# Kernel optimization log

Measured on AMD Instinct MI355X. Metric: run time of the kernel, lower is better.

## Reference

```python
import jax, jax.numpy as jnp
import numpy as np

N_TOKENS = 4096
HIDDEN = 2048
INTER = 1024
N_EXPERTS = 8          # routed experts
ZERO_EXPERTS = 2       # Longcat zero-computation (identity) experts
TOP_K = 2
ROUTED_SCALING = 2.5


def setup_inputs() -> dict:
    key = jax.random.key(0)
    k1, k2, k3, k4 = jax.random.split(key, 4)
    hidden_states = jax.random.normal(k1, (N_TOKENS, HIDDEN), dtype=jnp.float32)
    router_w = jax.random.normal(k2, (N_EXPERTS + ZERO_EXPERTS, HIDDEN), dtype=jnp.float32) * 0.02
    correction_bias = jnp.zeros((N_EXPERTS + ZERO_EXPERTS,), dtype=jnp.float32)
    # torch Linear weight layout [out, in]: gate_up [E, 2I, H], down [E, H, I]
    w_gate_up = jax.random.normal(k3, (N_EXPERTS, 2 * INTER, HIDDEN), dtype=jnp.float32) * 0.02
    w_down = jax.random.normal(k4, (N_EXPERTS, HIDDEN, INTER), dtype=jnp.float32) * 0.02
    return {
        'hidden_states': hidden_states,
        'router_w': router_w,
        'correction_bias': correction_bias,
        'w_gate_up': w_gate_up,
        'w_down': w_down,
    }


def reference(hidden_states, router_w, correction_bias, w_gate_up, w_down):
    x = hidden_states  # [N, H]
    # ---- router gemm (fp32, like dsv3_router_gemm) ----
    logits = jnp.einsum('nh,eh->ne', x.astype(jnp.float32), router_w)  # [N, E+Z]
    scores = jax.nn.sigmoid(logits)
    # biased top-k selection (sglang biased topk, renormalize=False)
    _, topk_idx = jax.lax.top_k(scores + correction_bias[None, :], TOP_K)  # [N, K]
    topk_w = jnp.take_along_axis(scores, topk_idx, axis=1)  # raw sigmoid scores
    # ---- combine weights per expert ----
    onehot = jax.nn.one_hot(topk_idx, N_EXPERTS + ZERO_EXPERTS, dtype=topk_w.dtype)  # [N,K,E+Z]
    combine = jnp.einsum('nke,nk->ne', onehot, topk_w)  # [N, E+Z]
    combine_real = combine[:, :N_EXPERTS]               # [N, E]
    w_zero = combine[:, N_EXPERTS:].sum(axis=-1)        # [N] identity-expert weight
    # ---- expert FFN (silu(gate) * up -> down), dense over experts ----
    gu = jnp.einsum('nh,efh->enf', x, w_gate_up)        # [E, N, 2I]
    gate, up = gu[..., :INTER], gu[..., INTER:]
    h = jax.nn.silu(gate) * up                          # [E, N, I]
    y = jnp.einsum('eni,ehi->enh', h, w_down)           # [E, N, H]
    out = jnp.einsum('enh,ne->nh', y, combine_real.astype(y.dtype))
    out = out + w_zero[:, None].astype(out.dtype) * x   # zero experts = identity
    return out * ROUTED_SCALING
```

## Files before the change

kernel.cpp:

```cpp
#include <hip/hip_runtime.h>
#include <cstdint>
#include <cstddef>

#define N_TOKENS 4096
#define HIDDEN   2048
#define INTER    1024
#define NE       8
#define NE_TOT   10
#define SCALE    2.5f

typedef short v8s __attribute__((ext_vector_type(8)));
typedef float v4f __attribute__((ext_vector_type(4)));

static __device__ inline int imin(int a, int b) { return a < b ? a : b; }

__device__ inline unsigned short f2bf(float f) {
  unsigned int u = __float_as_uint(f);
  u += 0x7fffu + ((u >> 16) & 1u);
  return (unsigned short)(u >> 16);
}

__device__ inline void gld_lds16(const void* g, void* l) {
  __builtin_amdgcn_global_load_lds(
      (const __attribute__((address_space(1))) unsigned int*)g,
      (__attribute__((address_space(3))) unsigned int*)l, 16, 0, 0);
}

__global__ void init_kernel(int* counts) {
  if (threadIdx.x < NE) counts[threadIdx.x] = 0;
}

__global__ __launch_bounds__(256) void cvt_kernel(const float* __restrict__ src,
                                                  unsigned short* __restrict__ dst,
                                                  int n8) {
  int i = blockIdx.x * 256 + threadIdx.x;
  if (i >= n8) return;
  size_t b = (size_t)i * 8;
  float4 a0 = *(const float4*)(src + b);
  float4 a1 = *(const float4*)(src + b + 4);
  union { unsigned short u[8]; uint4 v; } r;
  r.u[0] = f2bf(a0.x); r.u[1] = f2bf(a0.y); r.u[2] = f2bf(a0.z); r.u[3] = f2bf(a0.w);
  r.u[4] = f2bf(a1.x); r.u[5] = f2bf(a1.y); r.u[6] = f2bf(a1.z); r.u[7] = f2bf(a1.w);
  *(uint4*)(dst + b) = r.v;
}

__global__ __launch_bounds__(256, 4) void router_kernel(
    const float* __restrict__ x, const float* __restrict__ rw,
    const float* __restrict__ bias, unsigned short* __restrict__ xb,
    int* __restrict__ counts, int* __restrict__ tok_list,
    float* __restrict__ tok_w, float* __restrict__ out) {
  int tid  = threadIdx.x;
  int lane = tid & 63;
  int wid  = tid >> 6;
  int n    = blockIdx.x * 4 + wid;

  const float* xr = x + (size_t)n * HIDDEN;
  float acc[NE_TOT];
#pragma unroll
  for (int e = 0; e < NE_TOT; e++) acc[e] = 0.f;

#pragma unroll 1
  for (int i = 0; i < 8; i++) {
    int k = (i * 64 + lane) * 4;
    float4 xv = *(const float4*)(xr + k);
#pragma unroll
    for (int e = 0; e < NE_TOT; e++) {
      float4 w = *(const float4*)(rw + (size_t)e * HIDDEN + k);
      acc[e] += xv.x * w.x + xv.y * w.y + xv.z * w.z + xv.w * w.w;
    }
  }
#pragma unroll
  for (int e = 0; e < NE_TOT; e++) {
    float v = acc[e];
#pragma unroll
    for (int off = 32; off > 0; off >>= 1) v += __shfl_xor(v, off, 64);
    acc[e] = v;
  }

  float sc[NE_TOT], sb[NE_TOT];
#pragma unroll
  for (int e = 0; e < NE_TOT; e++) {
    sc[e] = 1.f / (1.f + expf(-acc[e]));
    sb[e] = sc[e] + bias[e];
  }
  int i1 = 0;
  for (int e = 1; e < NE_TOT; e++) if (sb[e] > sb[i1]) i1 = e;
  int i2 = (i1 == 0) ? 1 : 0;
  for (int e = 0; e < NE_TOT; e++) if (e != i1 && sb[e] > sb[i2]) i2 = e;
  float wzero = 0.f;
  if (i1 >= NE) wzero += sc[i1];
  if (i2 >= NE) wzero += sc[i2];
  if (lane == 0) {
#pragma unroll
    for (int tt = 0; tt < 2; tt++) {
      int idx = tt == 0 ? i1 : i2;
      if (idx < NE) {
        int slot = atomicAdd(&counts[idx], 1);
        tok_list[idx * N_TOKENS + slot] = n;
        tok_w[idx * N_TOKENS + slot]    = SCALE * sc[idx];
      }
    }
  }
  float wz = SCALE * wzero;

#pragma unroll
  for (int i = 0; i < 8; i++) {
    int k = (i * 64 + lane) * 4;
    float4 xv = *(const float4*)(xr + k);
    ushort4 ob;
    ob.x = f2bf(xv.x); ob.y = f2bf(xv.y);
    ob.z = f2bf(xv.z); ob.w = f2bf(xv.w);
    *(ushort4*)(xb + (size_t)n * HIDDEN + k) = ob;
    float4 o;
    o.x = wz * xv.x; o.y = wz * xv.y; o.z = wz * xv.z; o.w = wz * xv.w;
    *(float4*)(out + (size_t)n * HIDDEN + k) = o;
  }
}

__global__ void offsets_kernel(const int* __restrict__ counts, int* __restrict__ offsets) {
  if (threadIdx.x == 0) {
    int s = 0;
    for (int e = 0; e < NE; e++) { offsets[e] = s; s += counts[e]; }
  }
}


__global__ __launch_bounds__(256, 2) void gateup_kernel(
    const unsigned short* __restrict__ xb, const unsigned short* __restrict__ wgu,
    const int* __restrict__ counts, const int* __restrict__ offsets,
    const int* __restrict__ tok_list, unsigned short* __restrict__ h_buf) {
  int jt = blockIdx.x;
  int mt = blockIdx.y;
  int e  = blockIdx.z;
  int count = counts[e];
  if (mt * 128 >= count) return;

  __shared__ unsigned short As[2][128 * 32];
  __shared__ unsigned short Bs[2][128 * 32];

  int tid  = threadIdx.x;
  int lane = tid & 63;
  int wm = (tid >> 7) & 1;
  int wn = (tid >> 6) & 1;

  int row0 = tid >> 2, row1 = row0 + 64;
  int col8 = (((tid & 3) ^ ((tid >> 3) & 3)) * 8);

  const int* tl = tok_list + e * N_TOKENS;
  int t0 = tl[imin(mt * 128 + row0, count - 1)];
  int t1 = tl[imin(mt * 128 + row1, count - 1)];
  const unsigned short* ag0 = xb + (size_t)t0 * HIDDEN + col8;
  const unsigned short* ag1 = xb + (size_t)t1 * HIDDEN + col8;

  int wn0 = row0 >> 6, wi0 = row0 & 63;
  int wn1 = row1 >> 6, wi1 = row1 & 63;
  int br0 = (wi0 < 32) ? (jt * 64 + wn0 * 32 + wi0) : (1024 + jt * 64 + wn0 * 32 + (wi0 - 32));
  int br1 = (wi1 < 32) ? (jt * 64 + wn1 * 32 + wi1) : (1024 + jt * 64 + wn1 * 32 + (wi1 - 32));
  const unsigned short* bbase = wgu + (size_t)e * (2 * INTER) * HIDDEN;
  const unsigned short* bg0 = bbase + (size_t)br0 * HIDDEN + col8;
  const unsigned short* bg1 = bbase + (size_t)br1 * HIDDEN + col8;

  v4f acc[4][4];
#pragma unroll
  for (int i = 0; i < 4; i++)
#pragma unroll
    for (int j = 0; j < 4; j++) acc[i][j] = v4f{0.f, 0.f, 0.f, 0.f};

  int mrow = wm * 64 + (lane & 15);
  int nrow = wn * 64 + (lane & 15);
  int kcol = (((lane >> 4) ^ ((lane >> 1) & 3)) * 8);

  gld_lds16(ag0, &As[0][(size_t)tid * 8]);
  gld_lds16(ag1, &As[0][2048 + (size_t)tid * 8]);
  gld_lds16(bg0, &Bs[0][(size_t)tid * 8]);
  gld_lds16(bg1, &Bs[0][2048 + (size_t)tid * 8]);
  ag0 += 32; ag1 += 32; bg0 += 32; bg1 += 32;
  __syncthreads();

  const int NK = HIDDEN / 32;
  for (int kt = 0; kt < NK; kt++) {
    int cur = kt & 1;
    if (kt + 1 < NK) {
      int nxt = cur ^ 1;
      gld_lds16(ag0, &As[nxt][(size_t)tid * 8]);
      gld_lds16(ag1, &As[nxt][2048 + (size_t)tid * 8]);
      gld_lds16(bg0, &Bs[nxt][(size_t)tid * 8]);
      gld_lds16(bg1, &Bs[nxt][2048 + (size_t)tid * 8]);
      ag0 += 32; ag1 += 32; bg0 += 32; bg1 += 32;
    }
    v8s a[4], b[4];
#pragma unroll
    for (int i = 0; i < 4; i++) a[i] = *(const v8s*)&As[cur][(mrow + i * 16) * 32 + kcol];
#pragma unroll
    for (int j = 0; j < 4; j++) b[j] = *(const v8s*)&Bs[cur][(nrow + j * 16) * 32 + kcol];
#pragma unroll
    for (int i = 0; i < 4; i++)
#pragma unroll
      for (int j = 0; j < 4; j++)
        acc[i][j] = __builtin_amdgcn_mfma_f32_16x16x32_bf16(a[i], b[j], acc[i][j], 0, 0, 0);
    __syncthreads();
  }

  int ocol  = lane & 15;
  int orow4 = (lane >> 4) * 4;
  int hoff  = offsets[e];
#pragma unroll
  for (int i = 0; i < 4; i++) {
#pragma unroll
    for (int r = 0; r < 4; r++) {
      int m = mt * 128 + wm * 64 + i * 16 + orow4 + r;
      if (m < count) {
        unsigned short* hrow = h_buf + (size_t)(hoff + m) * INTER;
#pragma unroll
        for (int j = 0; j < 2; j++) {
          float g = acc[i][j][r];
          float u = acc[i][j + 2][r];
          float hv = (g / (1.f + expf(-g))) * u;
          hrow[jt * 64 + wn * 32 + j * 16 + ocol] = f2bf(hv);
        }
      }
    }
  }
}

__global__ __launch_bounds__(256, 2) void down_kernel(
    const unsigned short* __restrict__ h_buf, const unsigned short* __restrict__ wd,
    const int* __restrict__ counts, const int* __restrict__ offsets,
    const int* __restrict__ tok_list, const float* __restrict__ tok_w,
    float* __restrict__ out) {
  int nt = blockIdx.x;
  int mt = blockIdx.y;
  int e  = blockIdx.z;
  int count = counts[e];
  if (mt * 128 >= count) return;

  __shared__ unsigned short As[2][128 * 32];
  __shared__ unsigned short Bs[2][128 * 32];

  int tid  = threadIdx.x;
  int lane = tid & 63;
  int wm = (tid >> 7) & 1;
  int wn = (tid >> 6) & 1;

  int row0 = tid >> 2, row1 = row0 + 64;
  int col8 = (((tid & 3) ^ ((tid >> 3) & 3)) * 8);
  int hoff = offsets[e];

  const unsigned short* ag0 =
      h_buf + (size_t)(hoff + imin(mt * 128 + row0, count - 1)) * INTER + col8;
  const unsigned short* ag1 =
      h_buf + (size_t)(hoff + imin(mt * 128 + row1, count - 1)) * INTER + col8;
  const unsigned short* bbase = wd + (size_t)e * HIDDEN * INTER;
  const unsigned short* bg0 = bbase + (size_t)(nt * 128 + row0) * INTER + col8;
  const unsigned short* bg1 = bbase + (size_t)(nt * 128 + row1) * INTER + col8;

  v4f acc[4][4];
#pragma unroll
  for (int i = 0; i < 4; i++)
#pragma unroll
    for (int j = 0; j < 4; j++) acc[i][j] = v4f{0.f, 0.f, 0.f, 0.f};

  int mrow = wm * 64 + (lane & 15);
  int nrow = wn * 64 + (lane & 15);
  int kcol = (((lane >> 4) ^ ((lane >> 1) & 3)) * 8);

  gld_lds16(ag0, &As[0][(size_t)tid * 8]);
  gld_lds16(ag1, &As[0][2048 + (size_t)tid * 8]);
  gld_lds16(bg0, &Bs[0][(size_t)tid * 8]);
  gld_lds16(bg1, &Bs[0][2048 + (size_t)tid * 8]);
  ag0 += 32; ag1 += 32; bg0 += 32; bg1 += 32;
  __syncthreads();

  const int NK = INTER / 32;
  for (int kt = 0; kt < NK; kt++) {
    int cur = kt & 1;
    if (kt + 1 < NK) {
      int nxt = cur ^ 1;
      gld_lds16(ag0, &As[nxt][(size_t)tid * 8]);
      gld_lds16(ag1, &As[nxt][2048 + (size_t)tid * 8]);
      gld_lds16(bg0, &Bs[nxt][(size_t)tid * 8]);
      gld_lds16(bg1, &Bs[nxt][2048 + (size_t)tid * 8]);
      ag0 += 32; ag1 += 32; bg0 += 32; bg1 += 32;
    }
    v8s a[4], b[4];
#pragma unroll
    for (int i = 0; i < 4; i++) a[i] = *(const v8s*)&As[cur][(mrow + i * 16) * 32 + kcol];
#pragma unroll
    for (int j = 0; j < 4; j++) b[j] = *(const v8s*)&Bs[cur][(nrow + j * 16) * 32 + kcol];
#pragma unroll
    for (int i = 0; i < 4; i++)
#pragma unroll
      for (int j = 0; j < 4; j++)
        acc[i][j] = __builtin_amdgcn_mfma_f32_16x16x32_bf16(a[i], b[j], acc[i][j], 0, 0, 0);
    __syncthreads();
  }

  int ocol  = lane & 15;
  int orow4 = (lane >> 4) * 4;
#pragma unroll
  for (int i = 0; i < 4; i++) {
#pragma unroll
    for (int r = 0; r < 4; r++) {
      int m = mt * 128 + wm * 64 + i * 16 + orow4 + r;
      if (m < count) {
        int tok  = tok_list[e * N_TOKENS + m];
        float w  = tok_w[e * N_TOKENS + m];
        float* orow = out + (size_t)tok * HIDDEN + nt * 128 + wn * 64 + ocol;
#pragma unroll
        for (int j = 0; j < 4; j++) atomicAdd(orow + j * 16, acc[i][j][r] * w);
      }
    }
  }
}

extern "C" void kernel_launch(void* const* d_in, const int* in_sizes, int n_in,
                              void* d_out, int out_size, void* d_ws, size_t ws_size,
                              hipStream_t stream) {
  const float* x   = (const float*)d_in[0];
  const float* rw  = (const float*)d_in[1];
  const float* cb  = (const float*)d_in[2];
  const float* wgu = (const float*)d_in[3];
  const float* wd  = (const float*)d_in[4];
  float* out = (float*)d_out;

  char* ws = (char*)d_ws;
  size_t off = 0;
  auto alloc = [&](size_t bytes) {
    void* p = ws + off;
    off += (bytes + 255) & ~(size_t)255;
    return p;
  };
  unsigned short* xb    = (unsigned short*)alloc((size_t)N_TOKENS * HIDDEN * 2);
  unsigned short* wgu_b = (unsigned short*)alloc((size_t)NE * 2 * INTER * HIDDEN * 2);
  unsigned short* wd_b  = (unsigned short*)alloc((size_t)NE * HIDDEN * INTER * 2);
  unsigned short* h_buf = (unsigned short*)alloc((size_t)2 * N_TOKENS * INTER * 2);
  int*   tok_list = (int*)alloc((size_t)NE * N_TOKENS * 4);
  float* tok_w    = (float*)alloc((size_t)NE * N_TOKENS * 4);
  int*   counts   = (int*)alloc(256);
  int*   offsets  = (int*)alloc(256);
  (void)ws_size; (void)in_sizes; (void)n_in; (void)out_size;

  init_kernel<<<1, 64, 0, stream>>>(counts);
  cvt_kernel<<<(NE * 2 * INTER * HIDDEN / 8 + 255) / 256, 256, 0, stream>>>(
      wgu, wgu_b, NE * 2 * INTER * HIDDEN / 8);
  cvt_kernel<<<(NE * HIDDEN * INTER / 8 + 255) / 256, 256, 0, stream>>>(
      wd, wd_b, NE * HIDDEN * INTER / 8);
  router_kernel<<<N_TOKENS / 4, 256, 0, stream>>>(x, rw, cb, xb, counts, tok_list, tok_w, out);
  offsets_kernel<<<1, 64, 0, stream>>>(counts, offsets);
  gateup_kernel<<<dim3(16, 32, 8), 256, 0, stream>>>(xb, wgu_b, counts, offsets, tok_list, h_buf);
  down_kernel<<<dim3(16, 32, 8), 256, 0, stream>>>(h_buf, wd_b, counts, offsets, tok_list, tok_w, out);
}
```

Measured before the change: 523.3 us.

## Replace down-proj atomic scatter with dense store plus per-token gather combine

The down-projection kernel now writes its fp32 results densely into a per-slot buffer (aliased onto the bf16 gate_up weight buffer, which is no longer needed by then) instead of issuing atomicAdd scatters into the output. A new gather kernel reads each token's two expert rows through packed (expert, slot) indices recorded by the router and adds the weighted sum to the output. The init and the two weight-conversion launches are merged into one kernel. This trades contended float atomics for an extra write and read of the intermediate buffer plus one more launch. If a token picks zero experts, its packed index of 0 makes the gather read a valid row with weight zero, which is harmless.

```diff
diff --git a/kernel.cpp b/kernel.cpp
--- a/kernel.cpp
+++ b/kernel.cpp
@@ -26,16 +26,20 @@
       (__attribute__((address_space(3))) unsigned int*)l, 16, 0, 0);
 }
 
-__global__ void init_kernel(int* counts) {
-  if (threadIdx.x < NE) counts[threadIdx.x] = 0;
-}
-
-__global__ __launch_bounds__(256) void cvt_kernel(const float* __restrict__ src,
-                                                  unsigned short* __restrict__ dst,
-                                                  int n8) {
+__global__ __launch_bounds__(256) void cvt_all_kernel(
+    const float* __restrict__ wgu, const float* __restrict__ wd,
+    unsigned short* __restrict__ wgu_b, unsigned short* __restrict__ wd_b,
+    int* __restrict__ counts) {
+  if (blockIdx.x == 0 && threadIdx.x < NE) counts[threadIdx.x] = 0;
   int i = blockIdx.x * 256 + threadIdx.x;
-  if (i >= n8) return;
-  size_t b = (size_t)i * 8;
+  const int n8_gu = NE * 2 * INTER * HIDDEN / 8;
+  const int n8_d  = NE * HIDDEN * INTER / 8;
+  const float* src;
+  unsigned short* dst;
+  size_t b;
+  if (i < n8_gu)            { src = wgu; dst = wgu_b; b = (size_t)i * 8; }
+  else if (i < n8_gu + n8_d){ src = wd;  dst = wd_b;  b = (size_t)(i - n8_gu) * 8; }
+  else return;
   float4 a0 = *(const float4*)(src + b);
   float4 a1 = *(const float4*)(src + b + 4);
   union { unsigned short u[8]; uint4 v; } r;
@@ -48,7 +52,7 @@
     const float* __restrict__ x, const float* __restrict__ rw,
     const float* __restrict__ bias, unsigned short* __restrict__ xb,
     int* __restrict__ counts, int* __restrict__ tok_list,
-    float* __restrict__ tok_w, float* __restrict__ out) {
+    int* __restrict__ tkp, float* __restrict__ tkw, float* __restrict__ out) {
   int tid  = threadIdx.x;
   int lane = tid & 63;
   int wid  = tid >> 6;
@@ -94,11 +98,16 @@
 #pragma unroll
     for (int tt = 0; tt < 2; tt++) {
       int idx = tt == 0 ? i1 : i2;
+      int packed = 0;
+      float w = 0.f;
       if (idx < NE) {
         int slot = atomicAdd(&counts[idx], 1);
         tok_list[idx * N_TOKENS + slot] = n;
-        tok_w[idx * N_TOKENS + slot]    = SCALE * sc[idx];
+        packed = (idx << 16) | slot;
+        w = SCALE * sc[idx];
       }
+      tkp[tt * N_TOKENS + n] = packed;
+      tkw[tt * N_TOKENS + n] = w;
     }
   }
   float wz = SCALE * wzero;
@@ -226,8 +235,7 @@
 __global__ __launch_bounds__(256, 2) void down_kernel(
     const unsigned short* __restrict__ h_buf, const unsigned short* __restrict__ wd,
     const int* __restrict__ counts, const int* __restrict__ offsets,
-    const int* __restrict__ tok_list, const float* __restrict__ tok_w,
-    float* __restrict__ out) {
+    float* __restrict__ y_buf) {
   int nt = blockIdx.x;
   int mt = blockIdx.y;
   int e  = blockIdx.z;
@@ -303,13 +311,40 @@
     for (int r = 0; r < 4; r++) {
       int m = mt * 128 + wm * 64 + i * 16 + orow4 + r;
       if (m < count) {
-        int tok  = tok_list[e * N_TOKENS + m];
-        float w  = tok_w[e * N_TOKENS + m];
-        float* orow = out + (size_t)tok * HIDDEN + nt * 128 + wn * 64 + ocol;
-#pragma unroll
-        for (int j = 0; j < 4; j++) atomicAdd(orow + j * 16, acc[i][j][r] * w);
+        float* yrow = y_buf + (size_t)(hoff + m) * HIDDEN + nt * 128 + wn * 64 + ocol;
+#pragma unroll
+        for (int j = 0; j < 4; j++) yrow[j * 16] = acc[i][j][r];
       }
     }
+  }
+}
+
+__global__ __launch_bounds__(256, 4) void gather_kernel(
+    const float* __restrict__ y_buf, const int* __restrict__ tkp,
+    const float* __restrict__ tkw, const int* __restrict__ offsets,
+    float* __restrict__ out) {
+  int tid  = threadIdx.x;
+  int lane = tid & 63;
+  int wid  = tid >> 6;
+  int n    = blockIdx.x * 4 + wid;
+
+  int p1 = tkp[n], p2 = tkp[N_TOKENS + n];
+  float w1 = tkw[n], w2 = tkw[N_TOKENS + n];
+  const float* y1 = y_buf + (size_t)(offsets[p1 >> 16] + (p1 & 0xffff)) * HIDDEN;
+  const float* y2 = y_buf + (size_t)(offsets[p2 >> 16] + (p2 & 0xffff)) * HIDDEN;
+  float* orow = out + (size_t)n * HIDDEN;
+
+#pragma unroll
+  for (int i = 0; i < 8; i++) {
+    int k = (i * 64 + lane) * 4;
+    float4 o = *(const float4*)(orow + k);
+    float4 a = *(const float4*)(y1 + k);
+    float4 b = *(const float4*)(y2 + k);
+    o.x += w1 * a.x + w2 * b.x;
+    o.y += w1 * a.y + w2 * b.y;
+    o.z += w1 * a.z + w2 * b.z;
+    o.w += w1 * a.w + w2 * b.w;
+    *(float4*)(orow + k) = o;
   }
 }
 
@@ -335,18 +370,18 @@
   unsigned short* wd_b  = (unsigned short*)alloc((size_t)NE * HIDDEN * INTER * 2);
   unsigned short* h_buf = (unsigned short*)alloc((size_t)2 * N_TOKENS * INTER * 2);
   int*   tok_list = (int*)alloc((size_t)NE * N_TOKENS * 4);
-  float* tok_w    = (float*)alloc((size_t)NE * N_TOKENS * 4);
+  int*   tkp      = (int*)alloc((size_t)2 * N_TOKENS * 4);
+  float* tkw      = (float*)alloc((size_t)2 * N_TOKENS * 4);
   int*   counts   = (int*)alloc(256);
   int*   offsets  = (int*)alloc(256);
+  float* y_buf = (float*)wgu_b;
   (void)ws_size; (void)in_sizes; (void)n_in; (void)out_size;
 
-  init_kernel<<<1, 64, 0, stream>>>(counts);
-  cvt_kernel<<<(NE * 2 * INTER * HIDDEN / 8 + 255) / 256, 256, 0, stream>>>(
-      wgu, wgu_b, NE * 2 * INTER * HIDDEN / 8);
-  cvt_kernel<<<(NE * HIDDEN * INTER / 8 + 255) / 256, 256, 0, stream>>>(
-      wd, wd_b, NE * HIDDEN * INTER / 8);
-  router_kernel<<<N_TOKENS / 4, 256, 0, stream>>>(x, rw, cb, xb, counts, tok_list, tok_w, out);
+  const int n8_total = (NE * 2 * INTER * HIDDEN + NE * HIDDEN * INTER) / 8;
+  cvt_all_kernel<<<(n8_total + 255) / 256, 256, 0, stream>>>(wgu, wd, wgu_b, wd_b, counts);
+  router_kernel<<<N_TOKENS / 4, 256, 0, stream>>>(x, rw, cb, xb, counts, tok_list, tkp, tkw, out);
   offsets_kernel<<<1, 64, 0, stream>>>(counts, offsets);
   gateup_kernel<<<dim3(16, 32, 8), 256, 0, stream>>>(xb, wgu_b, counts, offsets, tok_list, h_buf);
-  down_kernel<<<dim3(16, 32, 8), 256, 0, stream>>>(h_buf, wd_b, counts, offsets, tok_list, tok_w, out);
-}
+  down_kernel<<<dim3(16, 32, 8), 256, 0, stream>>>(h_buf, wd_b, counts, offsets, y_buf);
+  gather_kernel<<<N_TOKENS / 4, 256, 0, stream>>>(y_buf, tkp, tkw, offsets, out);
+}
```

Result: no change. 516.7 us (-1.3%).
